# Kernel optimization log

Measured on AMD Instinct MI355X. Metric: run time of the kernel, lower is better.

## Reference

```python
import jax, jax.numpy as jnp
import numpy as np

SOFTENING = 0.01
SOFTENING_SQ = SOFTENING * SOFTENING


def setup_inputs() -> dict:
    key = jax.random.key(0)
    k1, k2 = jax.random.split(key)
    N = 8192
    positions = jax.random.normal(k1, (N, 3), dtype=jnp.float32)
    masses = jax.random.uniform(k2, (N,), dtype=jnp.float32)
    return {"positions": positions, "masses": masses}


def reference(positions, masses):
    # diff[i, j] = r_j - r_i  -> shape (N, N, 3)
    diff = positions[None, :, :] - positions[:, None, :]
    dist_sq = jnp.sum(diff * diff, axis=2) + SOFTENING_SQ        # (N, N)
    inv_dist_cubed = dist_sq ** (-1.5)                            # (N, N)
    # a_i = sum_j m_j * diff[i, j] * inv_dist_cubed[i, j]
    w = masses[None, :] * inv_dist_cubed                          # (N, N)
    accelerations = jnp.einsum('ij,ijd->id', w, diff)             # (N, 3)
    return accelerations
```

## Files before the change

### kernel.cpp

```cpp
#include <hip/hip_runtime.h>

#define NBODY 8192
#define BLOCK 256
#define IPT 4
#define ITILE (BLOCK * IPT)
#define NITILES (NBODY / ITILE)
#define SLABS 128
#define JCHUNK (NBODY / SLABS)
#define PHASE 16
#define NPHASE (JCHUNK / PHASE)
#define NF (NBODY * 3)
#define SOFT2 1.0e-4f

__global__ __launch_bounds__(BLOCK, 4) void force_kernel(
    const float* __restrict__ pos, const float* __restrict__ mass,
    float* __restrict__ part) {
  __shared__ float4 tile[JCHUNK];

  const int t = threadIdx.x;
  const int j0 = blockIdx.y * JCHUNK;
  if (t < JCHUNK) {
    const int j = j0 + t;
    tile[t] =
        make_float4(pos[j * 3 + 0], pos[j * 3 + 1], pos[j * 3 + 2], mass[j]);
  }

  const int ib = blockIdx.x * ITILE + t;
  float xi[IPT], yi[IPT], zi[IPT];
  float ax[IPT], ay[IPT], az[IPT];
#pragma unroll
  for (int p = 0; p < IPT; ++p) {
    const int i = ib + p * BLOCK;
    xi[p] = pos[i * 3 + 0];
    yi[p] = pos[i * 3 + 1];
    zi[p] = pos[i * 3 + 2];
    ax[p] = 0.f;
    ay[p] = 0.f;
    az[p] = 0.f;
  }

  __syncthreads();

  for (int c = 0; c < NPHASE; ++c) {
    float4 jt[PHASE];
#pragma unroll
    for (int u = 0; u < PHASE; ++u) jt[u] = tile[c * PHASE + u];

#pragma unroll
    for (int u = 0; u < PHASE; ++u) {
#pragma unroll
      for (int p = 0; p < IPT; ++p) {
        float dx = jt[u].x - xi[p];
        float dy = jt[u].y - yi[p];
        float dz = jt[u].z - zi[p];
        float r2 = fmaf(dx, dx, fmaf(dy, dy, fmaf(dz, dz, SOFT2)));
        float inv = __builtin_amdgcn_rsqf(r2);
        float w = jt[u].w * (inv * inv * inv);
        ax[p] = fmaf(w, dx, ax[p]);
        ay[p] = fmaf(w, dy, ay[p]);
        az[p] = fmaf(w, dz, az[p]);
      }
    }
  }

  float* __restrict__ dst = part + (size_t)blockIdx.y * NF;
#pragma unroll
  for (int p = 0; p < IPT; ++p) {
    const int i = ib + p * BLOCK;
    dst[0 * NBODY + i] = ax[p];
    dst[1 * NBODY + i] = ay[p];
    dst[2 * NBODY + i] = az[p];
  }
}

__global__ __launch_bounds__(BLOCK) void reduce_kernel(
    const float* __restrict__ part, float* __restrict__ out) {
  const int idx = blockIdx.x * BLOCK + threadIdx.x;
  const int c = idx >> 13;
  const int b = idx & (NBODY - 1);
  const int sl0 = blockIdx.y * (SLABS / 4);
  float s0 = 0.f, s1 = 0.f, s2 = 0.f, s3 = 0.f;
#pragma unroll 8
  for (int sl = 0; sl < SLABS / 4; sl += 4) {
    s0 += part[(size_t)(sl0 + sl + 0) * NF + idx];
    s1 += part[(size_t)(sl0 + sl + 1) * NF + idx];
    s2 += part[(size_t)(sl0 + sl + 2) * NF + idx];
    s3 += part[(size_t)(sl0 + sl + 3) * NF + idx];
  }
  atomicAdd(&out[b * 3 + c], (s0 + s1) + (s2 + s3));
}

extern "C" void kernel_launch(void* const* d_in, const int* in_sizes, int n_in,
                              void* d_out, int out_size, void* d_ws,
                              size_t ws_size, hipStream_t stream) {
  const float* pos = (const float*)d_in[0];
  const float* mass = (const float*)d_in[1];
  float* out = (float*)d_out;
  float* part = (float*)d_ws;

  hipMemsetAsync(d_out, 0, (size_t)out_size * sizeof(float), stream);

  force_kernel<<<dim3(NITILES, SLABS), BLOCK, 0, stream>>>(pos, mass, part);
  reduce_kernel<<<dim3(NF / BLOCK, 4), BLOCK, 0, stream>>>(part, out);
}
```

Before: 82.94 us.

## Exploit force symmetry with wave-rotated j-bodies and atomic accumulation

Measured after the change: 84.19 us. About the same (+1.5%).

```diff
diff --git a/kernel.cpp b/kernel.cpp
--- a/kernel.cpp
+++ b/kernel.cpp
@@ -5,89 +5,122 @@
 #define IPT 4
 #define ITILE (BLOCK * IPT)
 #define NITILES (NBODY / ITILE)
-#define SLABS 128
-#define JCHUNK (NBODY / SLABS)
-#define PHASE 16
-#define NPHASE (JCHUNK / PHASE)
-#define NF (NBODY * 3)
+#define NGROUPS (NBODY / 64)
+#define GPT (ITILE / 64)
 #define SOFT2 1.0e-4f
 
-__global__ __launch_bounds__(BLOCK, 4) void force_kernel(
+__device__ __forceinline__ float rotf(int rotidx, float v) {
+  return __int_as_float(
+      __builtin_amdgcn_ds_bpermute(rotidx, __float_as_int(v)));
+}
+
+__global__ __launch_bounds__(BLOCK) void force_kernel(
     const float* __restrict__ pos, const float* __restrict__ mass,
-    float* __restrict__ part) {
-  __shared__ float4 tile[JCHUNK];
+    float* __restrict__ out) {
+  const int x = blockIdx.x;
+  const int g = blockIdx.y;
+  if (g < x * GPT) return;
+  const bool sym = (g >= (x + 1) * GPT);
+
+  __shared__ float jmerge[BLOCK / 64][64][3];
 
   const int t = threadIdx.x;
-  const int j0 = blockIdx.y * JCHUNK;
-  if (t < JCHUNK) {
-    const int j = j0 + t;
-    tile[t] =
-        make_float4(pos[j * 3 + 0], pos[j * 3 + 1], pos[j * 3 + 2], mass[j]);
-  }
+  const int lane = t & 63;
+  const int wv = t >> 6;
+  const int jbase = g * 64;
+  const int ibase = x * ITILE;
 
-  const int ib = blockIdx.x * ITILE + t;
-  float xi[IPT], yi[IPT], zi[IPT];
+  float xi[IPT], yi[IPT], zi[IPT], mi[IPT];
   float ax[IPT], ay[IPT], az[IPT];
 #pragma unroll
   for (int p = 0; p < IPT; ++p) {
-    const int i = ib + p * BLOCK;
+    const int i = ibase + p * BLOCK + t;
     xi[p] = pos[i * 3 + 0];
     yi[p] = pos[i * 3 + 1];
     zi[p] = pos[i * 3 + 2];
+    mi[p] = mass[i];
     ax[p] = 0.f;
     ay[p] = 0.f;
     az[p] = 0.f;
   }
 
-  __syncthreads();
+  const int j = jbase + lane;
+  float jx = pos[j * 3 + 0];
+  float jy = pos[j * 3 + 1];
+  float jz = pos[j * 3 + 2];
+  float jm = mass[j];
+  float jax = 0.f, jay = 0.f, jaz = 0.f;
 
-  for (int c = 0; c < NPHASE; ++c) {
-    float4 jt[PHASE];
-#pragma unroll
-    for (int u = 0; u < PHASE; ++u) jt[u] = tile[c * PHASE + u];
+  const int rotidx = ((lane + 1) & 63) * 4;
 
-#pragma unroll
-    for (int u = 0; u < PHASE; ++u) {
+  if (sym) {
+#pragma unroll 2
+    for (int s = 0; s < 64; ++s) {
 #pragma unroll
       for (int p = 0; p < IPT; ++p) {
-        float dx = jt[u].x - xi[p];
-        float dy = jt[u].y - yi[p];
-        float dz = jt[u].z - zi[p];
+        float dx = jx - xi[p];
+        float dy = jy - yi[p];
+        float dz = jz - zi[p];
         float r2 = fmaf(dx, dx, fmaf(dy, dy, fmaf(dz, dz, SOFT2)));
         float inv = __builtin_amdgcn_rsqf(r2);
-        float w = jt[u].w * (inv * inv * inv);
+        float inv3 = (inv * inv) * inv;
+        float wi = jm * inv3;
+        float wj = mi[p] * inv3;
+        ax[p] = fmaf(wi, dx, ax[p]);
+        ay[p] = fmaf(wi, dy, ay[p]);
+        az[p] = fmaf(wi, dz, az[p]);
+        jax = fmaf(-wj, dx, jax);
+        jay = fmaf(-wj, dy, jay);
+        jaz = fmaf(-wj, dz, jaz);
+      }
+      jx = rotf(rotidx, jx);
+      jy = rotf(rotidx, jy);
+      jz = rotf(rotidx, jz);
+      jm = rotf(rotidx, jm);
+      jax = rotf(rotidx, jax);
+      jay = rotf(rotidx, jay);
+      jaz = rotf(rotidx, jaz);
+    }
+
+    jmerge[wv][lane][0] = jax;
+    jmerge[wv][lane][1] = jay;
+    jmerge[wv][lane][2] = jaz;
+    __syncthreads();
+    if (t < 64 * 3) {
+      const int jl = t / 3, c = t % 3;
+      float s = jmerge[0][jl][c] + jmerge[1][jl][c] + jmerge[2][jl][c] +
+                jmerge[3][jl][c];
+      atomicAdd(&out[(jbase + jl) * 3 + c], s);
+    }
+  } else {
+#pragma unroll 2
+    for (int s = 0; s < 64; ++s) {
+#pragma unroll
+      for (int p = 0; p < IPT; ++p) {
+        float dx = jx - xi[p];
+        float dy = jy - yi[p];
+        float dz = jz - zi[p];
+        float r2 = fmaf(dx, dx, fmaf(dy, dy, fmaf(dz, dz, SOFT2)));
+        float inv = __builtin_amdgcn_rsqf(r2);
+        float w = jm * ((inv * inv) * inv);
         ax[p] = fmaf(w, dx, ax[p]);
         ay[p] = fmaf(w, dy, ay[p]);
         az[p] = fmaf(w, dz, az[p]);
       }
+      jx = rotf(rotidx, jx);
+      jy = rotf(rotidx, jy);
+      jz = rotf(rotidx, jz);
+      jm = rotf(rotidx, jm);
     }
   }
 
-  float* __restrict__ dst = part + (size_t)blockIdx.y * NF;
 #pragma unroll
   for (int p = 0; p < IPT; ++p) {
-    const int i = ib + p * BLOCK;
-    dst[0 * NBODY + i] = ax[p];
-    dst[1 * NBODY + i] = ay[p];
-    dst[2 * NBODY + i] = az[p];
+    const int i = ibase + p * BLOCK + t;
+    atomicAdd(&out[i * 3 + 0], ax[p]);
+    atomicAdd(&out[i * 3 + 1], ay[p]);
+    atomicAdd(&out[i * 3 + 2], az[p]);
   }
-}
-
-__global__ __launch_bounds__(BLOCK) void reduce_kernel(
-    const float* __restrict__ part, float* __restrict__ out) {
-  const int idx = blockIdx.x * BLOCK + threadIdx.x;
-  const int c = idx >> 13;
-  const int b = idx & (NBODY - 1);
-  const int sl0 = blockIdx.y * (SLABS / 4);
-  float s0 = 0.f, s1 = 0.f, s2 = 0.f, s3 = 0.f;
-#pragma unroll 8
-  for (int sl = 0; sl < SLABS / 4; sl += 4) {
-    s0 += part[(size_t)(sl0 + sl + 0) * NF + idx];
-    s1 += part[(size_t)(sl0 + sl + 1) * NF + idx];
-    s2 += part[(size_t)(sl0 + sl + 2) * NF + idx];
-    s3 += part[(size_t)(sl0 + sl + 3) * NF + idx];
-  }
-  atomicAdd(&out[b * 3 + c], (s0 + s1) + (s2 + s3));
 }
 
 extern "C" void kernel_launch(void* const* d_in, const int* in_sizes, int n_in,
@@ -96,10 +129,8 @@
   const float* pos = (const float*)d_in[0];
   const float* mass = (const float*)d_in[1];
   float* out = (float*)d_out;
-  float* part = (float*)d_ws;
 
   hipMemsetAsync(d_out, 0, (size_t)out_size * sizeof(float), stream);
 
-  force_kernel<<<dim3(NITILES, SLABS), BLOCK, 0, stream>>>(pos, mass, part);
-  reduce_kernel<<<dim3(NF / BLOCK, 4), BLOCK, 0, stream>>>(part, out);
+  force_kernel<<<dim3(NITILES, NGROUPS), BLOCK, 0, stream>>>(pos, mass, out);
 }
```

## Expand squared distance algebraically and replace partial-sum reduce with direct atomics

Applied to the files above, without the earlier changes.

After: 95.47 us. +15.1%, slower.

```diff
diff --git a/kernel.cpp b/kernel.cpp
--- a/kernel.cpp
+++ b/kernel.cpp
@@ -7,87 +7,76 @@
 #define NITILES (NBODY / ITILE)
 #define SLABS 128
 #define JCHUNK (NBODY / SLABS)
-#define PHASE 16
+#define PHASE 8
 #define NPHASE (JCHUNK / PHASE)
-#define NF (NBODY * 3)
 #define SOFT2 1.0e-4f
 
 __global__ __launch_bounds__(BLOCK, 4) void force_kernel(
     const float* __restrict__ pos, const float* __restrict__ mass,
-    float* __restrict__ part) {
+    float* __restrict__ out) {
   __shared__ float4 tile[JCHUNK];
+  __shared__ float jn[JCHUNK];
 
   const int t = threadIdx.x;
-  const int j0 = blockIdx.y * JCHUNK;
   if (t < JCHUNK) {
-    const int j = j0 + t;
-    tile[t] =
-        make_float4(pos[j * 3 + 0], pos[j * 3 + 1], pos[j * 3 + 2], mass[j]);
+    const int j = blockIdx.y * JCHUNK + t;
+    const float jx = pos[j * 3 + 0];
+    const float jy = pos[j * 3 + 1];
+    const float jz = pos[j * 3 + 2];
+    tile[t] = make_float4(-2.f * jx, -2.f * jy, -2.f * jz, -0.5f * mass[j]);
+    jn[t] = fmaf(jx, jx, fmaf(jy, jy, jz * jz));
   }
 
   const int ib = blockIdx.x * ITILE + t;
-  float xi[IPT], yi[IPT], zi[IPT];
-  float ax[IPT], ay[IPT], az[IPT];
+  float xi[IPT], yi[IPT], zi[IPT], ni[IPT];
+  float ax[IPT], ay[IPT], az[IPT], sw[IPT];
 #pragma unroll
   for (int p = 0; p < IPT; ++p) {
     const int i = ib + p * BLOCK;
     xi[p] = pos[i * 3 + 0];
     yi[p] = pos[i * 3 + 1];
     zi[p] = pos[i * 3 + 2];
-    ax[p] = 0.f;
-    ay[p] = 0.f;
-    az[p] = 0.f;
+    ni[p] = fmaf(xi[p], xi[p],
+                 fmaf(yi[p], yi[p], fmaf(zi[p], zi[p], SOFT2)));
+    ax[p] = 0.f; ay[p] = 0.f; az[p] = 0.f; sw[p] = 0.f;
   }
 
   __syncthreads();
 
   for (int c = 0; c < NPHASE; ++c) {
     float4 jt[PHASE];
+    float jv[PHASE];
 #pragma unroll
-    for (int u = 0; u < PHASE; ++u) jt[u] = tile[c * PHASE + u];
+    for (int u = 0; u < PHASE; ++u) {
+      jt[u] = tile[c * PHASE + u];
+      jv[u] = jn[c * PHASE + u];
+    }
 
 #pragma unroll
     for (int u = 0; u < PHASE; ++u) {
 #pragma unroll
       for (int p = 0; p < IPT; ++p) {
-        float dx = jt[u].x - xi[p];
-        float dy = jt[u].y - yi[p];
-        float dz = jt[u].z - zi[p];
-        float r2 = fmaf(dx, dx, fmaf(dy, dy, fmaf(dz, dz, SOFT2)));
-        float inv = __builtin_amdgcn_rsqf(r2);
-        float w = jt[u].w * (inv * inv * inv);
-        ax[p] = fmaf(w, dx, ax[p]);
-        ay[p] = fmaf(w, dy, ay[p]);
-        az[p] = fmaf(w, dz, az[p]);
+        float r2 = fmaf(jt[u].x, xi[p],
+                   fmaf(jt[u].y, yi[p],
+                   fmaf(jt[u].z, zi[p], jv[u] + ni[p])));
+        float y = __builtin_amdgcn_rsqf(r2);
+        float W = jt[u].w * ((y * y) * y);
+        ax[p] = fmaf(W, jt[u].x, ax[p]);
+        ay[p] = fmaf(W, jt[u].y, ay[p]);
+        az[p] = fmaf(W, jt[u].z, az[p]);
+        sw[p] += W;
       }
     }
   }
 
-  float* __restrict__ dst = part + (size_t)blockIdx.y * NF;
 #pragma unroll
   for (int p = 0; p < IPT; ++p) {
     const int i = ib + p * BLOCK;
-    dst[0 * NBODY + i] = ax[p];
-    dst[1 * NBODY + i] = ay[p];
-    dst[2 * NBODY + i] = az[p];
+    const float s2 = sw[p] + sw[p];
+    atomicAdd(&out[i * 3 + 0], fmaf(s2, xi[p], ax[p]));
+    atomicAdd(&out[i * 3 + 1], fmaf(s2, yi[p], ay[p]));
+    atomicAdd(&out[i * 3 + 2], fmaf(s2, zi[p], az[p]));
   }
-}
-
-__global__ __launch_bounds__(BLOCK) void reduce_kernel(
-    const float* __restrict__ part, float* __restrict__ out) {
-  const int idx = blockIdx.x * BLOCK + threadIdx.x;
-  const int c = idx >> 13;
-  const int b = idx & (NBODY - 1);
-  const int sl0 = blockIdx.y * (SLABS / 4);
-  float s0 = 0.f, s1 = 0.f, s2 = 0.f, s3 = 0.f;
-#pragma unroll 8
-  for (int sl = 0; sl < SLABS / 4; sl += 4) {
-    s0 += part[(size_t)(sl0 + sl + 0) * NF + idx];
-    s1 += part[(size_t)(sl0 + sl + 1) * NF + idx];
-    s2 += part[(size_t)(sl0 + sl + 2) * NF + idx];
-    s3 += part[(size_t)(sl0 + sl + 3) * NF + idx];
-  }
-  atomicAdd(&out[b * 3 + c], (s0 + s1) + (s2 + s3));
 }
 
 extern "C" void kernel_launch(void* const* d_in, const int* in_sizes, int n_in,
@@ -96,10 +85,8 @@
   const float* pos = (const float*)d_in[0];
   const float* mass = (const float*)d_in[1];
   float* out = (float*)d_out;
-  float* part = (float*)d_ws;
 
   hipMemsetAsync(d_out, 0, (size_t)out_size * sizeof(float), stream);
 
-  force_kernel<<<dim3(NITILES, SLABS), BLOCK, 0, stream>>>(pos, mass, part);
-  reduce_kernel<<<dim3(NF / BLOCK, 4), BLOCK, 0, stream>>>(part, out);
+  force_kernel<<<dim3(NITILES, SLABS), BLOCK, 0, stream>>>(pos, mass, out);
 }
```
